# Optimization experiments

Hardware: AMD Instinct MI355X
Metric: run time of the kernel (lower is better)

Reference implementation:

```python
import jax, jax.numpy as jnp
import numpy as np

B, D = 1, 128
N_STATE, N_EULER, N_FIELD = 4, 3, 1
BUF = 1  # filter_nb // 2


def setup_inputs() -> dict:
    key = jax.random.key(0)
    k1, k2, k3, k4 = jax.random.split(key, 4)
    state0 = jax.random.randint(k1, (B, D, D, D), 0, N_STATE).astype(jnp.float32)
    euler0 = jax.random.uniform(k2, (B, D, D, D, 3), dtype=jnp.float32)
    field0 = jax.random.uniform(k3, (B, D, D, D, 1), dtype=jnp.float32)
    x = jnp.concatenate([state0[..., None], euler0, field0], axis=-1)  # [B,D,D,D,5]
    out = jax.random.normal(k4, (B, D, D, D, N_STATE + N_EULER + N_FIELD), dtype=jnp.float32)
    return {"x": x, "out": out}


def _gather_neighbors(euler0):
    # euler0: [B,D,D,D,3] -> [B,D,D,D,26,3] via 26 fixed shifts (zero-padded, non-periodic)
    d = euler0.shape[1]
    pad = jnp.pad(euler0, ((0, 0), (BUF, BUF), (BUF, BUF), (BUF, BUF), (0, 0)))
    slices = []
    for di in (-1, 0, 1):
        for dj in (-1, 0, 1):
            for dk in (-1, 0, 1):
                if di == 0 and dj == 0 and dk == 0:
                    continue
                slices.append(pad[:, BUF + di:BUF + di + d,
                                  BUF + dj:BUF + dj + d,
                                  BUF + dk:BUF + dk + d, :])
    return jnp.stack(slices, axis=4)


def reference(x, out):
    # Cafe_RNN.decode with n_euler=3 (get_rot is identity).
    state0 = x[..., 0].astype(jnp.int32)                       # [B,D,D,D]
    state1 = jnp.argmax(out[..., :N_STATE], axis=-1).astype(jnp.int32)
    state1 = jnp.where(state0 == 0, 0, state1)

    field1 = out[..., -N_FIELD:]                               # [B,D,D,D,1]
    m_le1 = (state1 <= 1)[..., None]
    m_eq2 = (state1 == 2)[..., None]
    m_eq3 = (state1 == 3)[..., None]
    field1 = jnp.where(m_le1, -1.0, field1)
    field1 = jnp.where(m_eq2, jnp.clip(field1, 0.0, 0.92), field1)
    field1 = jnp.where(m_eq3, 1.0, field1)

    euler1 = x[..., 1:4]
    euler1 = jnp.where(m_le1, -1.0, euler1)

    # Solidification: for cells that just solidified, snap euler to the nearest
    # neighbor euler (min squared distance to the predicted rotation rot1).
    flag_solidify = jnp.logical_and(state0 <= 1, state1 > 1)   # [B,D,D,D]
    rot0_nbs = _gather_neighbors(x[..., 1:4])                  # [B,D,D,D,26,3]
    rot1 = out[..., N_STATE:N_STATE + N_EULER]                 # [B,D,D,D,3]
    dist = jnp.sum(jnp.square(rot0_nbs - rot1[..., None, :]), axis=-1)  # [B,D,D,D,26]
    imin = jnp.argmin(dist, axis=-1)                           # [B,D,D,D]
    chosen = jnp.take_along_axis(rot0_nbs, imin[..., None, None], axis=4)[..., 0, :]
    euler1 = jnp.where(flag_solidify[..., None], chosen, euler1)

    state1f = jax.lax.stop_gradient(state1.astype(x.dtype))
    return jnp.concatenate([state1f[..., None], euler1, field1], axis=-1)
```

## Files before the change

kernel.cpp:

```cpp
#include <hip/hip_runtime.h>

#pragma clang fp contract(off)

#define DD 128
#define NCELL (DD * DD * DD)
#define CPT 4
#define NWAVE (NCELL / 256)

__device__ __forceinline__ void nbr_off(int m, int& di, int& dj, int& dk) {
    const int idx = (m < 13) ? m : m + 1;
    di = idx / 9 - 1;
    dj = (idx / 3) % 3 - 1;
    dk = idx % 3 - 1;
}

__global__ __launch_bounds__(256) void k1_dense(
    const float* __restrict__ x,
    const float* __restrict__ out,
    float* __restrict__ y,
    int* __restrict__ wcnt,
    int* __restrict__ list)
{
    const int t  = blockIdx.x * blockDim.x + threadIdx.x;
    const int n0 = t * CPT;
    if (n0 >= NCELL) return;

    const int w    = t >> 6;
    const int lane = threadIdx.x & 63;
    const unsigned long long lt = (1ull << lane) - 1ull;

    float4 xa[5], oa[8];
    const float4* xp = reinterpret_cast<const float4*>(x) + (size_t)t * 5;
    const float4* op = reinterpret_cast<const float4*>(out) + (size_t)t * 8;
#pragma unroll
    for (int q = 0; q < 5; ++q) xa[q] = xp[q];
#pragma unroll
    for (int q = 0; q < 8; ++q) oa[q] = op[q];

    float xv[20], ov[32], rv[20];
#pragma unroll
    for (int q = 0; q < 5; ++q) {
        xv[q * 4 + 0] = xa[q].x; xv[q * 4 + 1] = xa[q].y;
        xv[q * 4 + 2] = xa[q].z; xv[q * 4 + 3] = xa[q].w;
    }
#pragma unroll
    for (int q = 0; q < 8; ++q) {
        ov[q * 4 + 0] = oa[q].x; ov[q * 4 + 1] = oa[q].y;
        ov[q * 4 + 2] = oa[q].z; ov[q * 4 + 3] = oa[q].w;
    }

    unsigned total = 0;

#pragma unroll
    for (int c = 0; c < CPT; ++c) {
        const int s0 = (int)xv[c * 5 + 0];

        float b = ov[c * 8 + 0];
        int   s1 = 0;
        if (ov[c * 8 + 1] > b) { b = ov[c * 8 + 1]; s1 = 1; }
        if (ov[c * 8 + 2] > b) { b = ov[c * 8 + 2]; s1 = 2; }
        if (ov[c * 8 + 3] > b) { b = ov[c * 8 + 3]; s1 = 3; }
        if (s0 == 0) s1 = 0;

        float f1 = ov[c * 8 + 7];
        float e0 = xv[c * 5 + 1], e1 = xv[c * 5 + 2], e2 = xv[c * 5 + 3];

        if (s1 <= 1) {
            f1 = -1.0f; e0 = -1.0f; e1 = -1.0f; e2 = -1.0f;
        } else if (s1 == 2) {
            f1 = fminf(fmaxf(f1, 0.0f), 0.92f);
        } else {
            f1 = 1.0f;
        }

        const bool flag = (s0 <= 1 && s1 > 1);
        const unsigned long long mask = __ballot(flag);
        if (flag) {
            const int pos = (int)total + (int)__popcll(mask & lt);
            list[(w << 8) + pos] = n0 + c;
        }
        total += (unsigned)__popcll(mask);

        rv[c * 5 + 0] = (float)s1;
        rv[c * 5 + 1] = e0;
        rv[c * 5 + 2] = e1;
        rv[c * 5 + 3] = e2;
        rv[c * 5 + 4] = f1;
    }

    if (lane == 0) wcnt[w] = (int)total;

    float4* yp = reinterpret_cast<float4*>(y) + (size_t)t * 5;
#pragma unroll
    for (int q = 0; q < 5; ++q) {
        float4 v;
        v.x = rv[q * 4 + 0]; v.y = rv[q * 4 + 1];
        v.z = rv[q * 4 + 2]; v.w = rv[q * 4 + 3];
        yp[q] = v;
    }
}

__global__ __launch_bounds__(256) void k2_gather(
    const float* __restrict__ x,
    const float* __restrict__ out,
    float* __restrict__ y,
    const int* __restrict__ wcnt,
    const int* __restrict__ list)
{
    const int seg = blockIdx.x;
    const int cnt = wcnt[seg];

    for (int i = threadIdx.x; i < cnt; i += 256) {
        const int n  = list[(seg << 8) + i];
        const int k  = n & (DD - 1);
        const int j  = (n >> 7) & (DD - 1);
        const int i0 = n >> 14;

        const float4 rot = *reinterpret_cast<const float4*>(out + (size_t)n * 8 + 4);
        const double r0 = (double)rot.x, r1 = (double)rot.y, r2 = (double)rot.z;

        float av[26][3];
#pragma unroll
        for (int m = 0; m < 26; ++m) {
            int di, dj, dk;
            nbr_off(m, di, dj, dk);
            const int ii = i0 + di, jj = j + dj, kk = k + dk;
            av[m][0] = 0.0f; av[m][1] = 0.0f; av[m][2] = 0.0f;
            if ((unsigned)ii < (unsigned)DD &&
                (unsigned)jj < (unsigned)DD &&
                (unsigned)kk < (unsigned)DD) {
                const float* p = x + ((size_t)((ii * DD + jj) * DD + kk)) * 5 + 1;
                av[m][0] = p[0]; av[m][1] = p[1]; av[m][2] = p[2];
            }
        }

        double best = 1.0e300;
        float ce0 = 0.0f, ce1 = 0.0f, ce2 = 0.0f;
#pragma unroll
        for (int m = 0; m < 26; ++m) {
            const double d0 = (double)av[m][0] - r0;
            const double d1 = (double)av[m][1] - r1;
            const double d2 = (double)av[m][2] - r2;
            const double dist = d0 * d0 + d1 * d1 + d2 * d2;
            if (dist < best) { best = dist; ce0 = av[m][0]; ce1 = av[m][1]; ce2 = av[m][2]; }
        }

        float* yp = y + (size_t)n * 5;
        yp[1] = ce0; yp[2] = ce1; yp[3] = ce2;
    }
}

__global__ __launch_bounds__(256) void cafe_rnn_fallback(
    const float* __restrict__ x,
    const float* __restrict__ out,
    float* __restrict__ y)
{
    const int t  = blockIdx.x * blockDim.x + threadIdx.x;
    const int n0 = t * CPT;
    if (n0 >= NCELL) return;

    float4 xa[5], oa[8];
    const float4* xp = reinterpret_cast<const float4*>(x) + (size_t)t * 5;
    const float4* op = reinterpret_cast<const float4*>(out) + (size_t)t * 8;
#pragma unroll
    for (int q = 0; q < 5; ++q) xa[q] = xp[q];
#pragma unroll
    for (int q = 0; q < 8; ++q) oa[q] = op[q];

    float xv[20], ov[32], rv[20];
#pragma unroll
    for (int q = 0; q < 5; ++q) {
        xv[q * 4 + 0] = xa[q].x; xv[q * 4 + 1] = xa[q].y;
        xv[q * 4 + 2] = xa[q].z; xv[q * 4 + 3] = xa[q].w;
    }
#pragma unroll
    for (int q = 0; q < 8; ++q) {
        ov[q * 4 + 0] = oa[q].x; ov[q * 4 + 1] = oa[q].y;
        ov[q * 4 + 2] = oa[q].z; ov[q * 4 + 3] = oa[q].w;
    }

#pragma unroll
    for (int c = 0; c < CPT; ++c) {
        const int s0 = (int)xv[c * 5 + 0];
        float b = ov[c * 8 + 0];
        int   s1 = 0;
        if (ov[c * 8 + 1] > b) { b = ov[c * 8 + 1]; s1 = 1; }
        if (ov[c * 8 + 2] > b) { b = ov[c * 8 + 2]; s1 = 2; }
        if (ov[c * 8 + 3] > b) { b = ov[c * 8 + 3]; s1 = 3; }
        if (s0 == 0) s1 = 0;

        float f1 = ov[c * 8 + 7];
        float e0 = xv[c * 5 + 1], e1 = xv[c * 5 + 2], e2 = xv[c * 5 + 3];
        if (s1 <= 1) { f1 = -1.0f; e0 = -1.0f; e1 = -1.0f; e2 = -1.0f; }
        else if (s1 == 2) { f1 = fminf(fmaxf(f1, 0.0f), 0.92f); }
        else { f1 = 1.0f; }

        if (s0 <= 1 && s1 > 1) {
            const int n = n0 + c;
            const int k = n & (DD - 1);
            const int j = (n >> 7) & (DD - 1);
            const int i = (n >> 14);
            const double r0 = (double)ov[c * 8 + 4];
            const double r1 = (double)ov[c * 8 + 5];
            const double r2 = (double)ov[c * 8 + 6];
            double best = 1.0e300;
            float ce0 = 0.0f, ce1 = 0.0f, ce2 = 0.0f;
#pragma unroll
            for (int m = 0; m < 26; ++m) {
                int di, dj, dk;
                nbr_off(m, di, dj, dk);
                const int ii = i + di, jj = j + dj, kk = k + dk;
                float a0 = 0.0f, a1 = 0.0f, a2 = 0.0f;
                if ((unsigned)ii < (unsigned)DD &&
                    (unsigned)jj < (unsigned)DD &&
                    (unsigned)kk < (unsigned)DD) {
                    const float* p = x + ((size_t)((ii * DD + jj) * DD + kk)) * 5 + 1;
                    a0 = p[0]; a1 = p[1]; a2 = p[2];
                }
                const double d0 = (double)a0 - r0;
                const double d1 = (double)a1 - r1;
                const double d2 = (double)a2 - r2;
                const double dist = d0 * d0 + d1 * d1 + d2 * d2;
                if (dist < best) { best = dist; ce0 = a0; ce1 = a1; ce2 = a2; }
            }
            e0 = ce0; e1 = ce1; e2 = ce2;
        }

        rv[c * 5 + 0] = (float)s1;
        rv[c * 5 + 1] = e0;
        rv[c * 5 + 2] = e1;
        rv[c * 5 + 3] = e2;
        rv[c * 5 + 4] = f1;
    }

    float4* yp = reinterpret_cast<float4*>(y) + (size_t)t * 5;
#pragma unroll
    for (int q = 0; q < 5; ++q) {
        float4 v;
        v.x = rv[q * 4 + 0]; v.y = rv[q * 4 + 1];
        v.z = rv[q * 4 + 2]; v.w = rv[q * 4 + 3];
        yp[q] = v;
    }
}

extern "C" void kernel_launch(void* const* d_in, const int* in_sizes, int n_in,
                              void* d_out, int out_size, void* d_ws, size_t ws_size,
                              hipStream_t stream) {
    const float* x   = (const float*)d_in[0];
    const float* out = (const float*)d_in[1];
    float* y = (float*)d_out;

    const int threads = 256;
    const int blocks1 = NCELL / (threads * CPT);

    const size_t need = (size_t)NWAVE * sizeof(int) + (size_t)NCELL * sizeof(int);
    if (ws_size >= need) {
        int* wcnt = (int*)d_ws;
        int* list = (int*)((char*)d_ws + (size_t)NWAVE * sizeof(int));
        k1_dense<<<blocks1, threads, 0, stream>>>(x, out, y, wcnt, list);
        k2_gather<<<NWAVE, threads, 0, stream>>>(x, out, y, wcnt, list);
    } else {
        cafe_rnn_fallback<<<blocks1, threads, 0, stream>>>(x, out, y);
    }
}
```

Before: 167.4 us.

## Split neighbor search across lane pairs and map one segment per wave

The gather kernel now assigns one compaction segment per wavefront and splits each solidifying cell's 26-neighbor search across two lanes of 13 neighbors each. The lanes combine their minima via shuffles with first-index tie-breaking. This raises lane utilisation and halves per-thread register arrays, at the cost of extra shuffles and a loop over 32-cell chunks. The dense kernel also moves the ballot and list compaction after the output stores.

```diff
diff --git a/kernel.cpp b/kernel.cpp
--- a/kernel.cpp
+++ b/kernel.cpp
@@ -25,10 +25,6 @@
     const int n0 = t * CPT;
     if (n0 >= NCELL) return;
 
-    const int w    = t >> 6;
-    const int lane = threadIdx.x & 63;
-    const unsigned long long lt = (1ull << lane) - 1ull;
-
     float4 xa[5], oa[8];
     const float4* xp = reinterpret_cast<const float4*>(x) + (size_t)t * 5;
     const float4* op = reinterpret_cast<const float4*>(out) + (size_t)t * 8;
@@ -49,8 +45,7 @@
         ov[q * 4 + 2] = oa[q].z; ov[q * 4 + 3] = oa[q].w;
     }
 
-    unsigned total = 0;
-
+    int fmask = 0;
 #pragma unroll
     for (int c = 0; c < CPT; ++c) {
         const int s0 = (int)xv[c * 5 + 0];
@@ -73,13 +68,7 @@
             f1 = 1.0f;
         }
 
-        const bool flag = (s0 <= 1 && s1 > 1);
-        const unsigned long long mask = __ballot(flag);
-        if (flag) {
-            const int pos = (int)total + (int)__popcll(mask & lt);
-            list[(w << 8) + pos] = n0 + c;
-        }
-        total += (unsigned)__popcll(mask);
+        fmask |= (int)(s0 <= 1 && s1 > 1) << c;
 
         rv[c * 5 + 0] = (float)s1;
         rv[c * 5 + 1] = e0;
@@ -88,8 +77,6 @@
         rv[c * 5 + 4] = f1;
     }
 
-    if (lane == 0) wcnt[w] = (int)total;
-
     float4* yp = reinterpret_cast<float4*>(y) + (size_t)t * 5;
 #pragma unroll
     for (int q = 0; q < 5; ++q) {
@@ -98,6 +85,22 @@
         v.z = rv[q * 4 + 2]; v.w = rv[q * 4 + 3];
         yp[q] = v;
     }
+
+    const int w    = t >> 6;
+    const int lane = threadIdx.x & 63;
+    const unsigned long long lt = (1ull << lane) - 1ull;
+    unsigned total = 0;
+#pragma unroll
+    for (int c = 0; c < CPT; ++c) {
+        const bool flag = (fmask >> c) & 1;
+        const unsigned long long mask = __ballot(flag);
+        if (flag) {
+            const int pos = (int)total + (int)__popcll(mask & lt);
+            list[(w << 8) + pos] = n0 + c;
+        }
+        total += (unsigned)__popcll(mask);
+    }
+    if (lane == 0) wcnt[w] = (int)total;
 }
 
 __global__ __launch_bounds__(256) void k2_gather(
@@ -107,11 +110,17 @@
     const int* __restrict__ wcnt,
     const int* __restrict__ list)
 {
-    const int seg = blockIdx.x;
-    const int cnt = wcnt[seg];
-
-    for (int i = threadIdx.x; i < cnt; i += 256) {
-        const int n  = list[(seg << 8) + i];
+    const int wiw  = threadIdx.x >> 6;
+    const int seg  = (blockIdx.x << 2) + wiw;
+    const int lane = threadIdx.x & 63;
+    const int half = lane & 1;
+    const int cnt  = wcnt[seg];
+
+    for (int base = 0; base < cnt; base += 32) {
+        const int slot   = base + (lane >> 1);
+        const bool active = (slot < cnt);
+        const int n = active ? list[(seg << 8) + slot] : 0;
+
         const int k  = n & (DD - 1);
         const int j  = (n >> 7) & (DD - 1);
         const int i0 = n >> 14;
@@ -119,34 +128,43 @@
         const float4 rot = *reinterpret_cast<const float4*>(out + (size_t)n * 8 + 4);
         const double r0 = (double)rot.x, r1 = (double)rot.y, r2 = (double)rot.z;
 
-        float av[26][3];
-#pragma unroll
-        for (int m = 0; m < 26; ++m) {
+        float av[13][3];
+#pragma unroll
+        for (int m2 = 0; m2 < 13; ++m2) {
             int di, dj, dk;
-            nbr_off(m, di, dj, dk);
+            nbr_off(half * 13 + m2, di, dj, dk);
             const int ii = i0 + di, jj = j + dj, kk = k + dk;
-            av[m][0] = 0.0f; av[m][1] = 0.0f; av[m][2] = 0.0f;
+            av[m2][0] = 0.0f; av[m2][1] = 0.0f; av[m2][2] = 0.0f;
             if ((unsigned)ii < (unsigned)DD &&
                 (unsigned)jj < (unsigned)DD &&
                 (unsigned)kk < (unsigned)DD) {
                 const float* p = x + ((size_t)((ii * DD + jj) * DD + kk)) * 5 + 1;
-                av[m][0] = p[0]; av[m][1] = p[1]; av[m][2] = p[2];
+                av[m2][0] = p[0]; av[m2][1] = p[1]; av[m2][2] = p[2];
             }
         }
 
         double best = 1.0e300;
         float ce0 = 0.0f, ce1 = 0.0f, ce2 = 0.0f;
 #pragma unroll
-        for (int m = 0; m < 26; ++m) {
-            const double d0 = (double)av[m][0] - r0;
-            const double d1 = (double)av[m][1] - r1;
-            const double d2 = (double)av[m][2] - r2;
+        for (int m2 = 0; m2 < 13; ++m2) {
+            const double d0 = (double)av[m2][0] - r0;
+            const double d1 = (double)av[m2][1] - r1;
+            const double d2 = (double)av[m2][2] - r2;
             const double dist = d0 * d0 + d1 * d1 + d2 * d2;
-            if (dist < best) { best = dist; ce0 = av[m][0]; ce1 = av[m][1]; ce2 = av[m][2]; }
-        }
-
-        float* yp = y + (size_t)n * 5;
-        yp[1] = ce0; yp[2] = ce1; yp[3] = ce2;
+            if (dist < best) { best = dist; ce0 = av[m2][0]; ce1 = av[m2][1]; ce2 = av[m2][2]; }
+        }
+
+        const double obest = __shfl_xor(best, 1, 64);
+        const float  oe0   = __shfl_xor(ce0, 1, 64);
+        const float  oe1   = __shfl_xor(ce1, 1, 64);
+        const float  oe2   = __shfl_xor(ce2, 1, 64);
+        const bool take_other = half ? (obest <= best) : (obest < best);
+        if (take_other) { ce0 = oe0; ce1 = oe1; ce2 = oe2; }
+
+        if (active && half == 0) {
+            float* yp = y + (size_t)n * 5;
+            yp[1] = ce0; yp[2] = ce1; yp[3] = ce2;
+        }
     }
 }
 
@@ -258,7 +276,7 @@
         int* wcnt = (int*)d_ws;
         int* list = (int*)((char*)d_ws + (size_t)NWAVE * sizeof(int));
         k1_dense<<<blocks1, threads, 0, stream>>>(x, out, y, wcnt, list);
-        k2_gather<<<NWAVE, threads, 0, stream>>>(x, out, y, wcnt, list);
+        k2_gather<<<NWAVE / 4, threads, 0, stream>>>(x, out, y, wcnt, list);
     } else {
         cafe_rnn_fallback<<<blocks1, threads, 0, stream>>>(x, out, y);
     }
```

New measurement: 172.3 us. 2.9% more time.
